# Optimization experiments

Measured on AMD Instinct MI355X. Metric: run time of the kernel, lower is better.

## Reference

```python
import jax, jax.numpy as jnp
import numpy as np

N_NODES = 100000
N_EDGES = 625000
HIDDEN = 128
N_LAYERS = 4
NUM_GRAPHS = 512
INPUT_DIM = 28
EDGE_DIM = 4
OUT_DIM = 1


def setup_inputs() -> dict:
    key = jax.random.key(0)
    ks = jax.random.split(key, 16)
    x = jax.random.randint(ks[0], (N_NODES, 1), 0, INPUT_DIM)
    edge_index = jax.random.randint(ks[1], (2, N_EDGES), 0, N_NODES)
    edge_attr = jax.random.randint(ks[2], (N_EDGES,), 0, EDGE_DIM)
    batch = jnp.sort(jax.random.randint(ks[3], (N_NODES,), 0, NUM_GRAPHS))
    s = 1.0 / np.sqrt(HIDDEN)
    node_emb = jax.random.normal(ks[4], (INPUT_DIM, HIDDEN), jnp.float32)
    edge_emb = jax.random.normal(ks[5], (EDGE_DIM, HIDDEN), jnp.float32)
    conv_W1 = jax.random.normal(ks[6], (N_LAYERS, HIDDEN, HIDDEN), jnp.float32) * s
    conv_b1 = jnp.zeros((N_LAYERS, HIDDEN), jnp.float32)
    conv_W2 = jax.random.normal(ks[7], (N_LAYERS, HIDDEN, HIDDEN), jnp.float32) * s
    conv_b2 = jnp.zeros((N_LAYERS, HIDDEN), jnp.float32)
    mlp_W1 = jax.random.normal(ks[8], (HIDDEN, HIDDEN // 2), jnp.float32) * s
    mlp_b1 = jnp.zeros((HIDDEN // 2,), jnp.float32)
    mlp_W2 = jax.random.normal(ks[9], (HIDDEN // 2, HIDDEN // 4), jnp.float32) * (1.0 / np.sqrt(HIDDEN // 2))
    mlp_b2 = jnp.zeros((HIDDEN // 4,), jnp.float32)
    mlp_W3 = jax.random.normal(ks[10], (HIDDEN // 4, OUT_DIM), jnp.float32) * (1.0 / np.sqrt(HIDDEN // 4))
    mlp_b3 = jnp.zeros((OUT_DIM,), jnp.float32)
    return dict(x=x, edge_index=edge_index, edge_attr=edge_attr, batch=batch,
                node_emb=node_emb, edge_emb=edge_emb,
                conv_W1=conv_W1, conv_b1=conv_b1, conv_W2=conv_W2, conv_b2=conv_b2,
                mlp_W1=mlp_W1, mlp_b1=mlp_b1, mlp_W2=mlp_W2, mlp_b2=mlp_b2,
                mlp_W3=mlp_W3, mlp_b3=mlp_b3)


def reference(x, edge_index, edge_attr, batch, node_emb, edge_emb,
              conv_W1, conv_b1, conv_W2, conv_b2,
              mlp_W1, mlp_b1, mlp_W2, mlp_b2, mlp_W3, mlp_b3):
    h = node_emb[x[:, 0]]                    # [N, H] embedding lookup (x.squeeze(-1))
    _attr = edge_emb[edge_attr]              # computed in original forward but unused by GINConv
    src, dst = edge_index[0], edge_index[1]
    for l in range(N_LAYERS):
        # GINConv (eps=0): mlp((1+eps)*x + sum_{j->i} x_j)
        agg = jax.ops.segment_sum(h[src], dst, num_segments=N_NODES)  # [N, H]
        z = agg + h
        z = jax.nn.relu(z @ conv_W1[l] + conv_b1[l])
        h = z @ conv_W2[l] + conv_b2[l]
    g = jax.ops.segment_sum(h, batch, num_segments=NUM_GRAPHS)        # global_add_pool [G, H]
    g = jax.nn.relu(g @ mlp_W1 + mlp_b1)
    g = jax.nn.relu(g @ mlp_W2 + mlp_b2)
    return g @ mlp_W3 + mlp_b3               # [G, 1]
```

## Files before the change

kernel.cpp:

```cpp
#include <hip/hip_runtime.h>

#define N_NODES 100000
#define N_EDGES 625000
#define HIDDEN 128
#define NUM_GRAPHS 512
#define CAP 40
#define PADN 100096

#define BUILD_BLKS 2443
#define EMBED_BLKS 6250
#define WT_BLKS 64

typedef unsigned int uint;
typedef unsigned short ushort;
typedef short v8s __attribute__((ext_vector_type(8)));
typedef float v16f __attribute__((ext_vector_type(16)));

__device__ __forceinline__ float b2f_lo(uint u) { return __uint_as_float(u << 16); }
__device__ __forceinline__ float b2f_hi(uint u) { return __uint_as_float(u & 0xffff0000u); }
__device__ __forceinline__ uint f2b(float f) {
  uint u = __float_as_uint(f);
  return (u + 0x7fffu + ((u >> 16) & 1u)) >> 16;
}

__global__ __launch_bounds__(256) void prep_k(const int* __restrict__ src,
                                              const int* __restrict__ dst,
                                              int* __restrict__ cursor,
                                              int* __restrict__ slots,
                                              const int* __restrict__ x,
                                              const float* __restrict__ emb,
                                              ushort* __restrict__ h,
                                              const float* __restrict__ W1,
                                              const float* __restrict__ W2,
                                              ushort* __restrict__ Wt) {
  int blk = blockIdx.x;
  int tid = threadIdx.x;
  if (blk < BUILD_BLKS) {
    int e = blk * 256 + tid;
    if (e < N_EDGES) {
      int d = dst[e];
      int p = atomicAdd(&cursor[d], 1);
      if (p < CAP) slots[(size_t)d * CAP + p] = src[e];
    }
  } else if (blk < BUILD_BLKS + EMBED_BLKS) {
    int t = (blk - BUILD_BLKS) * 256 + tid;
    int n = t >> 4;
    if (n < N_NODES) {
      int c = t & 15;
      const float4* e4 = (const float4*)(emb + (size_t)x[n] * HIDDEN + c * 8);
      float4 a = e4[0], b = e4[1];
      uint4 o;
      o.x = f2b(a.x) | (f2b(a.y) << 16);
      o.y = f2b(a.z) | (f2b(a.w) << 16);
      o.z = f2b(b.x) | (f2b(b.y) << 16);
      o.w = f2b(b.z) | (f2b(b.w) << 16);
      ((uint4*)h)[t] = o;
    }
  } else {
    int wb = blk - BUILD_BLKS - EMBED_BLKS;
    int mat = wb >> 3, chunk = wb & 7;
    const float* W = ((mat & 1) ? W2 : W1) + (size_t)(mat >> 1) * 16384;
    ushort* o = Wt + (size_t)mat * 16384;
#pragma unroll
    for (int jj = 0; jj < 8; jj++) {
      int idx = chunk * 2048 + tid + 256 * jj;
      int k = idx >> 7, n = idx & 127;
      int c = n >> 5, l31 = n & 31;
      int ks = k >> 4, khalf = (k >> 3) & 1, e = k & 7;
      o[(((c * 8 + ks) << 6) + (khalf << 5) + l31) * 8 + e] = (ushort)f2b(W[idx]);
    }
  }
}

__global__ __launch_bounds__(256) void hist_k(const int* __restrict__ cursor,
                                              int* __restrict__ bins) {
  __shared__ int lb[CAP + 1];
  int tid = threadIdx.x;
  if (tid <= CAP) lb[tid] = 0;
  __syncthreads();
  int n = blockIdx.x * 256 + tid;
  if (n < N_NODES) {
    int d = cursor[n]; if (d > CAP) d = CAP;
    atomicAdd(&lb[d], 1);
  }
  __syncthreads();
  if (tid <= CAP && lb[tid] > 0) atomicAdd(&bins[tid], lb[tid]);
}

__global__ __launch_bounds__(64) void scan_k(int* __restrict__ bins) {
  int i = threadIdx.x;
  int c = (i <= CAP) ? bins[i] : 0;
  int incl = c;
#pragma unroll
  for (int off = 1; off < 64; off <<= 1) {
    int t = __shfl_up(incl, off, 64);
    if (i >= off) incl += t;
  }
  if (i <= CAP) bins[i] = incl - c;
}

__global__ __launch_bounds__(256) void scatter_k(const int* __restrict__ cursor,
                                                 int* __restrict__ bins,
                                                 int* __restrict__ perm) {
  __shared__ int lb[CAP + 1];
  __shared__ int lbase[CAP + 1];
  int tid = threadIdx.x;
  if (tid <= CAP) lb[tid] = 0;
  __syncthreads();
  int n = blockIdx.x * 256 + tid;
  int d = 0, rank = 0;
  bool real = (n < N_NODES);
  if (real) {
    d = cursor[n]; if (d > CAP) d = CAP;
    rank = atomicAdd(&lb[d], 1);
  }
  __syncthreads();
  if (tid <= CAP) {
    int c = lb[tid];
    lbase[tid] = c > 0 ? atomicAdd(&bins[tid], c) : 0;
  }
  __syncthreads();
  if (real) perm[(N_NODES - 1) - (lbase[d] + rank)] = n;
  else if (n < PADN) perm[n] = 0;
}

union U { uint4 u; v8s s; };

__device__ __forceinline__ void loadrow(uint4 dst[8], const uint4* __restrict__ rowp,
                                        int khalf) {
#pragma unroll
  for (int ks = 0; ks < 8; ks++) dst[ks] = rowp[khalf + 2 * ks];
}

__device__ __forceinline__ void accum8(const uint4 u[8], float acc[8][8]) {
#pragma unroll
  for (int ks = 0; ks < 8; ks++) {
    acc[ks][0] += b2f_lo(u[ks].x); acc[ks][1] += b2f_hi(u[ks].x);
    acc[ks][2] += b2f_lo(u[ks].y); acc[ks][3] += b2f_hi(u[ks].y);
    acc[ks][4] += b2f_lo(u[ks].z); acc[ks][5] += b2f_hi(u[ks].z);
    acc[ks][6] += b2f_lo(u[ks].w); acc[ks][7] += b2f_hi(u[ks].w);
  }
}

__global__ __launch_bounds__(64, 3) void layer_k(const ushort* __restrict__ hin,
                                                 const int* __restrict__ cursor,
                                                 const int* __restrict__ slots,
                                                 const int* __restrict__ perm,
                                                 const ushort* __restrict__ W1f,
                                                 const ushort* __restrict__ W2f,
                                                 const float* __restrict__ b1,
                                                 const float* __restrict__ b2,
                                                 ushort* __restrict__ hout) {
  int lane = threadIdx.x;
  int l31 = lane & 31;
  int khalf = lane >> 5;
  int tb = blockIdx.x * 32;
  int prow = perm[tb + l31];
  bool valid = (tb + l31) < N_NODES;

  float acc[8][8];
#pragma unroll
  for (int ks = 0; ks < 8; ks++)
#pragma unroll
    for (int e = 0; e < 8; e++) acc[ks][e] = 0.f;

  const uint4* base = (const uint4*)hin;
  uint4 A[8], B[8];
  loadrow(A, base + (size_t)prow * 16, khalf);

  int deg = valid ? cursor[prow] : 0;
  if (deg > CAP) deg = CAP;
  const int* sl = slots + (size_t)prow * CAP;
  if (deg > 0) loadrow(B, base + (size_t)sl[0] * 16, khalf);
  __builtin_amdgcn_sched_barrier(0);
  accum8(A, acc);

  int j = 0;
  while (j + 2 <= deg) {
    loadrow(A, base + (size_t)sl[j + 1] * 16, khalf);
    __builtin_amdgcn_sched_barrier(0);
    accum8(B, acc);
    if (j + 2 < deg) loadrow(B, base + (size_t)sl[j + 2] * 16, khalf);
    __builtin_amdgcn_sched_barrier(0);
    accum8(A, acc);
    j += 2;
  }
  if (j < deg) accum8(B, acc);

  U afr[8];
#pragma unroll
  for (int ks = 0; ks < 8; ks++) {
    afr[ks].u.x = f2b(acc[ks][0]) | (f2b(acc[ks][1]) << 16);
    afr[ks].u.y = f2b(acc[ks][2]) | (f2b(acc[ks][3]) << 16);
    afr[ks].u.z = f2b(acc[ks][4]) | (f2b(acc[ks][5]) << 16);
    afr[ks].u.w = f2b(acc[ks][6]) | (f2b(acc[ks][7]) << 16);
  }

  const uint4* W1v = (const uint4*)W1f;
  v16f acc1[4] = {};
#pragma unroll
  for (int c = 0; c < 4; c++)
#pragma unroll
    for (int ks = 0; ks < 8; ks++) {
      U b; b.u = W1v[((c * 8 + ks) << 6) + lane];
      acc1[c] = __builtin_amdgcn_mfma_f32_32x32x16_bf16(b.s, afr[ks].s, acc1[c], 0, 0, 0);
    }

  uint u[4][4][2];
#pragma unroll
  for (int c = 0; c < 4; c++)
#pragma unroll
    for (int b = 0; b < 4; b++)
#pragma unroll
      for (int ap = 0; ap < 2; ap++) {
        int r0 = 2 * ap + 4 * b, r1 = r0 + 1;
        float v0 = fmaxf(acc1[c][r0] + b1[c * 32 + 2 * ap + 8 * b + 4 * khalf], 0.f);
        float v1 = fmaxf(acc1[c][r1] + b1[c * 32 + 2 * ap + 1 + 8 * b + 4 * khalf], 0.f);
        u[c][b][ap] = f2b(v0) | (f2b(v1) << 16);
      }

  uint got[4][2][2];
#pragma unroll
  for (int c = 0; c < 4; c++)
#pragma unroll
    for (int bh = 0; bh < 2; bh++)
#pragma unroll
      for (int ap = 0; ap < 2; ap++) {
        uint send = khalf ? u[c][2 * bh][ap] : u[c][2 * bh + 1][ap];
        got[c][bh][ap] = __shfl_xor(send, 32, 64);
      }

  U az[8];
#pragma unroll
  for (int ks = 0; ks < 8; ks++) {
    uint o0 = khalf ? u[ks >> 1][2 * (ks & 1) + 1][0] : u[ks >> 1][2 * (ks & 1)][0];
    uint o1 = khalf ? u[ks >> 1][2 * (ks & 1) + 1][1] : u[ks >> 1][2 * (ks & 1)][1];
    uint g0 = got[ks >> 1][ks & 1][0];
    uint g1 = got[ks >> 1][ks & 1][1];
    az[ks].u.x = khalf ? g0 : o0;
    az[ks].u.y = khalf ? g1 : o1;
    az[ks].u.z = khalf ? o0 : g0;
    az[ks].u.w = khalf ? o1 : g1;
  }

  const uint4* W2v = (const uint4*)W2f;
  v16f acc2[4] = {};
#pragma unroll
  for (int c = 0; c < 4; c++)
#pragma unroll
    for (int ks = 0; ks < 8; ks++) {
      U b; b.u = W2v[((c * 8 + ks) << 6) + lane];
      acc2[c] = __builtin_amdgcn_mfma_f32_32x32x16_bf16(az[ks].s, b.s, acc2[c], 0, 0, 0);
    }

  int trow[16];
#pragma unroll
  for (int r = 0; r < 16; r++) {
    int m = (r & 3) + 8 * (r >> 2) + 4 * khalf;
    trow[r] = __shfl(prow, m, 64);
  }
  float bv2[4];
#pragma unroll
  for (int c = 0; c < 4; c++) bv2[c] = b2[c * 32 + l31];
#pragma unroll
  for (int c = 0; c < 4; c++) {
    int col = c * 32 + l31;
#pragma unroll
    for (int r = 0; r < 16; r++) {
      int m = (r & 3) + 8 * (r >> 2) + 4 * khalf;
      if (tb + m < N_NODES)
        hout[(size_t)trow[r] * HIDDEN + col] = (ushort)f2b(acc2[c][r] + bv2[c]);
    }
  }
}

__global__ __launch_bounds__(256) void poolmlp_k(const ushort* __restrict__ h,
                                                 const int* __restrict__ batch,
                                                 const float* __restrict__ W1, const float* __restrict__ b1,
                                                 const float* __restrict__ W2, const float* __restrict__ b2,
                                                 const float* __restrict__ W3, const float* __restrict__ b3,
                                                 float* __restrict__ out) {
  __shared__ int se[2];
  __shared__ float red[16][16][8];
  __shared__ float gl[128];
  __shared__ float r2[64];
  __shared__ float r3[32];
  int gi = blockIdx.x, tid = threadIdx.x;
  if (tid < 2) {
    int target = gi + tid;
    int lo = 0, hi = N_NODES;
    while (lo < hi) {
      int mid = (lo + hi) >> 1;
      if (batch[mid] < target) lo = mid + 1; else hi = mid;
    }
    se[tid] = lo;
  }
  __syncthreads();
  int start = se[0], end = se[1];
  int cg = tid & 15, rg = tid >> 4;
  float acc[8] = {0.f, 0.f, 0.f, 0.f, 0.f, 0.f, 0.f, 0.f};
  for (int r = start + rg; r < end; r += 16) {
    uint4 v = ((const uint4*)h)[r * 16 + cg];
    acc[0] += b2f_lo(v.x); acc[1] += b2f_hi(v.x);
    acc[2] += b2f_lo(v.y); acc[3] += b2f_hi(v.y);
    acc[4] += b2f_lo(v.z); acc[5] += b2f_hi(v.z);
    acc[6] += b2f_lo(v.w); acc[7] += b2f_hi(v.w);
  }
#pragma unroll
  for (int j = 0; j < 8; j++) red[rg][cg][j] = acc[j];
  __syncthreads();
  if (rg == 0) {
    float s[8];
#pragma unroll
    for (int j = 0; j < 8; j++) s[j] = red[0][cg][j];
#pragma unroll
    for (int i = 1; i < 16; i++)
#pragma unroll
      for (int j = 0; j < 8; j++) s[j] += red[i][cg][j];
#pragma unroll
    for (int j = 0; j < 8; j++) gl[cg * 8 + j] = s[j];
  }
  __syncthreads();
  if (tid < 64) {
    float s = b1[tid];
    for (int k = 0; k < 128; k++) s = fmaf(gl[k], W1[k * 64 + tid], s);
    r2[tid] = fmaxf(s, 0.f);
  }
  __syncthreads();
  if (tid < 32) {
    float s2 = b2[tid];
    for (int k = 0; k < 64; k++) s2 = fmaf(r2[k], W2[k * 32 + tid], s2);
    r3[tid] = fmaxf(s2, 0.f);
  }
  __syncthreads();
  if (tid < 64) {
    float pv = (tid < 32) ? r3[tid] * W3[tid] : 0.f;
#pragma unroll
    for (int off = 32; off > 0; off >>= 1) pv += __shfl_down(pv, off);
    if (tid == 0) out[gi] = pv + b3[0];
  }
}

extern "C" void kernel_launch(void* const* d_in, const int* in_sizes, int n_in,
                              void* d_out, int out_size, void* d_ws, size_t ws_size,
                              hipStream_t stream) {
  const int* x = (const int*)d_in[0];
  const int* src = (const int*)d_in[1];
  const int* dst = src + N_EDGES;
  const int* batch = (const int*)d_in[3];
  const float* node_emb = (const float*)d_in[4];
  const float* cW1 = (const float*)d_in[6];
  const float* cb1 = (const float*)d_in[7];
  const float* cW2 = (const float*)d_in[8];
  const float* cb2 = (const float*)d_in[9];
  const float* mW1 = (const float*)d_in[10];
  const float* mb1 = (const float*)d_in[11];
  const float* mW2 = (const float*)d_in[12];
  const float* mb2 = (const float*)d_in[13];
  const float* mW3 = (const float*)d_in[14];
  const float* mb3 = (const float*)d_in[15];
  float* out = (float*)d_out;

  char* p = (char*)d_ws;
  const size_t HB = (size_t)N_NODES * HIDDEN * sizeof(ushort);
  ushort* h = (ushort*)p;      p += HB;
  ushort* t0 = (ushort*)p;     p += HB;
  ushort* Wtb = (ushort*)p;    p += (size_t)8 * 16384 * sizeof(ushort);
  int* cursor = (int*)p;       p += (size_t)N_NODES * sizeof(int);
  int* bins = (int*)p;         p += 64 * sizeof(int);
  int* slots = (int*)p;        p += (size_t)N_NODES * CAP * sizeof(int);
  int* perm = (int*)p;         p += (size_t)PADN * sizeof(int);

  (void)hipMemsetAsync(cursor, 0, ((size_t)N_NODES + 64) * sizeof(int), stream);
  prep_k<<<BUILD_BLKS + EMBED_BLKS + WT_BLKS, 256, 0, stream>>>(
      src, dst, cursor, slots, x, node_emb, h, cW1, cW2, Wtb);
  hist_k<<<PADN / 256, 256, 0, stream>>>(cursor, bins);
  scan_k<<<1, 64, 0, stream>>>(bins);
  scatter_k<<<PADN / 256, 256, 0, stream>>>(cursor, bins, perm);

  const int grid = PADN / 32;
  ushort* bufs[2] = {h, t0};
  for (int l = 0; l < 4; l++) {
    layer_k<<<grid, 64, 0, stream>>>(bufs[l & 1], cursor, slots, perm,
                                     Wtb + (size_t)(2 * l) * 16384,
                                     Wtb + (size_t)(2 * l + 1) * 16384,
                                     cb1 + (size_t)l * HIDDEN,
                                     cb2 + (size_t)l * HIDDEN,
                                     bufs[(l & 1) ^ 1]);
  }
  poolmlp_k<<<NUM_GRAPHS, 256, 0, stream>>>(h, batch, mW1, mb1, mW2, mb2, mW3, mb3, out);
}
```

Baseline: 341.1 us.

## Split neighbor aggregation across two wavefronts with LDS reduction

The layer kernel now launches 128 threads per block: two wavefronts each gather alternate neighbors of the same 32 nodes, and the second wave's partial sums are reduced through shared memory before only the first wave runs the MFMA MLP. Neighbor slot indices are prefetched as int4 vectors instead of scalar loads. This is meant to halve the serial gather latency chain per node and raise memory-level parallelism. The costs are a 16KB LDS buffer, a block barrier, an idle second wave during the GEMM phase, and lower occupancy pressure trade-offs.

Result: slower. 563.7 us (+65.3%).

```diff
diff --git a/kernel.cpp b/kernel.cpp
--- a/kernel.cpp
+++ b/kernel.cpp
@@ -142,16 +142,19 @@
   }
 }
 
-__global__ __launch_bounds__(64, 3) void layer_k(const ushort* __restrict__ hin,
-                                                 const int* __restrict__ cursor,
-                                                 const int* __restrict__ slots,
-                                                 const int* __restrict__ perm,
-                                                 const ushort* __restrict__ W1f,
-                                                 const ushort* __restrict__ W2f,
-                                                 const float* __restrict__ b1,
-                                                 const float* __restrict__ b2,
-                                                 ushort* __restrict__ hout) {
-  int lane = threadIdx.x;
+__global__ __launch_bounds__(128, 4) void layer_k(const ushort* __restrict__ hin,
+                                                  const int* __restrict__ cursor,
+                                                  const int* __restrict__ slots,
+                                                  const int* __restrict__ perm,
+                                                  const ushort* __restrict__ W1f,
+                                                  const ushort* __restrict__ W2f,
+                                                  const float* __restrict__ b1,
+                                                  const float* __restrict__ b2,
+                                                  ushort* __restrict__ hout) {
+  __shared__ float red[64 * 64];
+  int tid = threadIdx.x;
+  int wid = tid >> 6;
+  int lane = tid & 63;
   int l31 = lane & 31;
   int khalf = lane >> 5;
   int tb = blockIdx.x * 32;
@@ -166,26 +169,64 @@
 
   const uint4* base = (const uint4*)hin;
   uint4 A[8], B[8];
-  loadrow(A, base + (size_t)prow * 16, khalf);
 
   int deg = valid ? cursor[prow] : 0;
   if (deg > CAP) deg = CAP;
-  const int* sl = slots + (size_t)prow * CAP;
-  if (deg > 0) loadrow(B, base + (size_t)sl[0] * 16, khalf);
-  __builtin_amdgcn_sched_barrier(0);
-  accum8(A, acc);
-
-  int j = 0;
-  while (j + 2 <= deg) {
-    loadrow(A, base + (size_t)sl[j + 1] * 16, khalf);
+  bool need2 = __ballot(deg > 1) != 0ull;
+
+  const int4* slv = (const int4*)(slots + (size_t)prow * CAP);
+  int mg = (deg - wid + 1) >> 1;
+  int4 ck = slv[0];
+  int4 cn = slv[1];
+
+  if (wid == 0) {
+    loadrow(A, base + (size_t)prow * 16, khalf);
+    if (mg > 0) loadrow(B, base + (size_t)ck.x * 16, khalf);
+    __builtin_amdgcn_sched_barrier(0);
+    accum8(A, acc);
+  } else {
+    if (mg > 0) loadrow(B, base + (size_t)ck.y * 16, khalf);
+    __builtin_amdgcn_sched_barrier(0);
+  }
+
+  int i = 0;
+  while (i + 2 <= mg) {
+    int sA = wid ? ck.w : ck.z;
+    loadrow(A, base + (size_t)sA * 16, khalf);
     __builtin_amdgcn_sched_barrier(0);
     accum8(B, acc);
-    if (j + 2 < deg) loadrow(B, base + (size_t)sl[j + 2] * 16, khalf);
+    int cidx = (i >> 1) + 2;
+    if (cidx > 9) cidx = 9;
+    int4 nx = slv[cidx];
+    if (i + 2 < mg) {
+      int sB = wid ? cn.y : cn.x;
+      loadrow(B, base + (size_t)sB * 16, khalf);
+    }
     __builtin_amdgcn_sched_barrier(0);
     accum8(A, acc);
-    j += 2;
-  }
-  if (j < deg) accum8(B, acc);
+    ck = cn; cn = nx;
+    i += 2;
+  }
+  if (i < mg) accum8(B, acc);
+
+  if (need2) {
+    if (wid == 1) {
+#pragma unroll
+      for (int ks = 0; ks < 8; ks++)
+#pragma unroll
+        for (int e = 0; e < 8; e++)
+          red[(ks * 8 + e) * 64 + lane] = acc[ks][e];
+    }
+    __syncthreads();
+    if (wid == 0) {
+#pragma unroll
+      for (int ks = 0; ks < 8; ks++)
+#pragma unroll
+        for (int e = 0; e < 8; e++)
+          acc[ks][e] += red[(ks * 8 + e) * 64 + lane];
+    }
+  }
+  if (wid == 1) return;
 
   U afr[8];
 #pragma unroll
@@ -381,12 +422,12 @@
   const int grid = PADN / 32;
   ushort* bufs[2] = {h, t0};
   for (int l = 0; l < 4; l++) {
-    layer_k<<<grid, 64, 0, stream>>>(bufs[l & 1], cursor, slots, perm,
-                                     Wtb + (size_t)(2 * l) * 16384,
-                                     Wtb + (size_t)(2 * l + 1) * 16384,
-                                     cb1 + (size_t)l * HIDDEN,
-                                     cb2 + (size_t)l * HIDDEN,
-                                     bufs[(l & 1) ^ 1]);
+    layer_k<<<grid, 128, 0, stream>>>(bufs[l & 1], cursor, slots, perm,
+                                      Wtb + (size_t)(2 * l) * 16384,
+                                      Wtb + (size_t)(2 * l + 1) * 16384,
+                                      cb1 + (size_t)l * HIDDEN,
+                                      cb2 + (size_t)l * HIDDEN,
+                                      bufs[(l & 1) ^ 1]);
   }
   poolmlp_k<<<NUM_GRAPHS, 256, 0, stream>>>(h, batch, mW1, mb1, mW2, mb2, mW3, mb3, out);
 }
```

## Split fused GIN layer into gather-aggregate kernel and in-place MLP GEMM kernel

Applied to the files above, without the earlier changes.

Each layer's fused gather+MLP kernel is split into two kernels. The new aggregation kernel puts 8 lanes on each node, each loading two 16-byte chunks, and prefetches neighbor indices as int4 with a four-deep pipeline of row loads. A separate GEMM kernel then reads the aggregated rows in natural order and writes the MLP output in place. This aims to improve memory-level parallelism and occupancy in the gather phase, at the cost of an extra write and read of the full node feature array and an extra launch per layer.

New measurement: 358.9 us. 5.2% more time.

```diff
diff --git a/kernel.cpp b/kernel.cpp
--- a/kernel.cpp
+++ b/kernel.cpp
@@ -126,15 +126,15 @@
 
 union U { uint4 u; v8s s; };
 
-__device__ __forceinline__ void loadrow(uint4 dst[8], const uint4* __restrict__ rowp,
-                                        int khalf) {
-#pragma unroll
-  for (int ks = 0; ks < 8; ks++) dst[ks] = rowp[khalf + 2 * ks];
-}
-
-__device__ __forceinline__ void accum8(const uint4 u[8], float acc[8][8]) {
-#pragma unroll
-  for (int ks = 0; ks < 8; ks++) {
+__device__ __forceinline__ void loadrow2(uint4 dst[2], const uint4* __restrict__ rowp,
+                                         int q) {
+  dst[0] = rowp[q];
+  dst[1] = rowp[q + 8];
+}
+
+__device__ __forceinline__ void accum2(const uint4 u[2], float acc[2][8]) {
+#pragma unroll
+  for (int ks = 0; ks < 2; ks++) {
     acc[ks][0] += b2f_lo(u[ks].x); acc[ks][1] += b2f_hi(u[ks].x);
     acc[ks][2] += b2f_lo(u[ks].y); acc[ks][3] += b2f_hi(u[ks].y);
     acc[ks][4] += b2f_lo(u[ks].z); acc[ks][5] += b2f_hi(u[ks].z);
@@ -142,59 +142,94 @@
   }
 }
 
-__global__ __launch_bounds__(64, 3) void layer_k(const ushort* __restrict__ hin,
-                                                 const int* __restrict__ cursor,
-                                                 const int* __restrict__ slots,
-                                                 const int* __restrict__ perm,
-                                                 const ushort* __restrict__ W1f,
-                                                 const ushort* __restrict__ W2f,
-                                                 const float* __restrict__ b1,
-                                                 const float* __restrict__ b2,
-                                                 ushort* __restrict__ hout) {
+__global__ __launch_bounds__(256, 5) void agg_k(const ushort* __restrict__ hin,
+                                                const int* __restrict__ cursor,
+                                                const int* __restrict__ slots,
+                                                const int* __restrict__ perm,
+                                                ushort* __restrict__ t1) {
+  int tid = threadIdx.x;
+  int lane = tid & 63;
+  int w = blockIdx.x * 4 + (tid >> 6);
+  int r8 = lane & 7;
+  int q = lane >> 3;
+  int pidx = w * 8 + r8;
+  bool valid = pidx < N_NODES;
+  int prow = valid ? perm[pidx] : 0;
+  int deg = valid ? cursor[prow] : 0;
+  if (deg > CAP) deg = CAP;
+  const int4* slv = (const int4*)(slots + (size_t)prow * CAP);
+  const uint4* base = (const uint4*)hin;
+
+  float acc[2][8];
+#pragma unroll
+  for (int ks = 0; ks < 2; ks++)
+#pragma unroll
+    for (int e = 0; e < 8; e++) acc[ks][e] = 0.f;
+
+  uint4 P0[2], P1[2], P2[2], P3[2];
+  int4 ck = slv[0];
+  int4 cn = slv[1];
+
+  loadrow2(P3, base + (size_t)prow * 16, q);
+  if (deg > 0) loadrow2(P0, base + (size_t)ck.x * 16, q);
+  if (deg > 1) loadrow2(P1, base + (size_t)ck.y * 16, q);
+  if (deg > 2) loadrow2(P2, base + (size_t)ck.z * 16, q);
+  __builtin_amdgcn_sched_barrier(0);
+  accum2(P3, acc);
+
+  int j = 0;
+  while (j + 4 <= deg) {
+    loadrow2(P3, base + (size_t)ck.w * 16, q);
+    __builtin_amdgcn_sched_barrier(0);
+    accum2(P0, acc);
+    int ni = (j >> 2) + 2; if (ni > 9) ni = 9;
+    int4 nx = slv[ni];
+    if (j + 4 < deg) loadrow2(P0, base + (size_t)cn.x * 16, q);
+    __builtin_amdgcn_sched_barrier(0);
+    accum2(P1, acc);
+    if (j + 5 < deg) loadrow2(P1, base + (size_t)cn.y * 16, q);
+    __builtin_amdgcn_sched_barrier(0);
+    accum2(P2, acc);
+    if (j + 6 < deg) loadrow2(P2, base + (size_t)cn.z * 16, q);
+    __builtin_amdgcn_sched_barrier(0);
+    accum2(P3, acc);
+    ck = cn; cn = nx;
+    j += 4;
+  }
+  if (j < deg)     accum2(P0, acc);
+  if (j + 1 < deg) accum2(P1, acc);
+  if (j + 2 < deg) accum2(P2, acc);
+
+  if (valid) {
+    uint4 o0, o1;
+    o0.x = f2b(acc[0][0]) | (f2b(acc[0][1]) << 16);
+    o0.y = f2b(acc[0][2]) | (f2b(acc[0][3]) << 16);
+    o0.z = f2b(acc[0][4]) | (f2b(acc[0][5]) << 16);
+    o0.w = f2b(acc[0][6]) | (f2b(acc[0][7]) << 16);
+    o1.x = f2b(acc[1][0]) | (f2b(acc[1][1]) << 16);
+    o1.y = f2b(acc[1][2]) | (f2b(acc[1][3]) << 16);
+    o1.z = f2b(acc[1][4]) | (f2b(acc[1][5]) << 16);
+    o1.w = f2b(acc[1][6]) | (f2b(acc[1][7]) << 16);
+    uint4* orow = (uint4*)(t1 + (size_t)prow * HIDDEN);
+    orow[q] = o0;
+    orow[q + 8] = o1;
+  }
+}
+
+__global__ __launch_bounds__(64, 3) void gemm_k(ushort* __restrict__ t,
+                                                const ushort* __restrict__ W1f,
+                                                const ushort* __restrict__ W2f,
+                                                const float* __restrict__ b1,
+                                                const float* __restrict__ b2) {
   int lane = threadIdx.x;
   int l31 = lane & 31;
   int khalf = lane >> 5;
-  int tb = blockIdx.x * 32;
-  int prow = perm[tb + l31];
-  bool valid = (tb + l31) < N_NODES;
-
-  float acc[8][8];
-#pragma unroll
-  for (int ks = 0; ks < 8; ks++)
-#pragma unroll
-    for (int e = 0; e < 8; e++) acc[ks][e] = 0.f;
-
-  const uint4* base = (const uint4*)hin;
-  uint4 A[8], B[8];
-  loadrow(A, base + (size_t)prow * 16, khalf);
-
-  int deg = valid ? cursor[prow] : 0;
-  if (deg > CAP) deg = CAP;
-  const int* sl = slots + (size_t)prow * CAP;
-  if (deg > 0) loadrow(B, base + (size_t)sl[0] * 16, khalf);
-  __builtin_amdgcn_sched_barrier(0);
-  accum8(A, acc);
-
-  int j = 0;
-  while (j + 2 <= deg) {
-    loadrow(A, base + (size_t)sl[j + 1] * 16, khalf);
-    __builtin_amdgcn_sched_barrier(0);
-    accum8(B, acc);
-    if (j + 2 < deg) loadrow(B, base + (size_t)sl[j + 2] * 16, khalf);
-    __builtin_amdgcn_sched_barrier(0);
-    accum8(A, acc);
-    j += 2;
-  }
-  if (j < deg) accum8(B, acc);
-
+  int rb = blockIdx.x * 32;
+
+  const uint4* rowp = (const uint4*)t + (size_t)(rb + l31) * 16;
   U afr[8];
 #pragma unroll
-  for (int ks = 0; ks < 8; ks++) {
-    afr[ks].u.x = f2b(acc[ks][0]) | (f2b(acc[ks][1]) << 16);
-    afr[ks].u.y = f2b(acc[ks][2]) | (f2b(acc[ks][3]) << 16);
-    afr[ks].u.z = f2b(acc[ks][4]) | (f2b(acc[ks][5]) << 16);
-    afr[ks].u.w = f2b(acc[ks][6]) | (f2b(acc[ks][7]) << 16);
-  }
+  for (int ks = 0; ks < 8; ks++) afr[ks].u = rowp[khalf + 2 * ks];
 
   const uint4* W1v = (const uint4*)W1f;
   v16f acc1[4] = {};
@@ -253,12 +288,6 @@
       acc2[c] = __builtin_amdgcn_mfma_f32_32x32x16_bf16(az[ks].s, b.s, acc2[c], 0, 0, 0);
     }
 
-  int trow[16];
-#pragma unroll
-  for (int r = 0; r < 16; r++) {
-    int m = (r & 3) + 8 * (r >> 2) + 4 * khalf;
-    trow[r] = __shfl(prow, m, 64);
-  }
   float bv2[4];
 #pragma unroll
   for (int c = 0; c < 4; c++) bv2[c] = b2[c * 32 + l31];
@@ -268,8 +297,7 @@
 #pragma unroll
     for (int r = 0; r < 16; r++) {
       int m = (r & 3) + 8 * (r >> 2) + 4 * khalf;
-      if (tb + m < N_NODES)
-        hout[(size_t)trow[r] * HIDDEN + col] = (ushort)f2b(acc2[c][r] + bv2[c]);
+      t[(size_t)(rb + m) * HIDDEN + col] = (ushort)f2b(acc2[c][r] + bv2[c]);
     }
   }
 }
@@ -378,15 +406,16 @@
   scan_k<<<1, 64, 0, stream>>>(bins);
   scatter_k<<<PADN / 256, 256, 0, stream>>>(cursor, bins, perm);
 
-  const int grid = PADN / 32;
   ushort* bufs[2] = {h, t0};
   for (int l = 0; l < 4; l++) {
-    layer_k<<<grid, 64, 0, stream>>>(bufs[l & 1], cursor, slots, perm,
-                                     Wtb + (size_t)(2 * l) * 16384,
-                                     Wtb + (size_t)(2 * l + 1) * 16384,
-                                     cb1 + (size_t)l * HIDDEN,
-                                     cb2 + (size_t)l * HIDDEN,
-                                     bufs[(l & 1) ^ 1]);
+    ushort* in = bufs[l & 1];
+    ushort* tmp = bufs[(l & 1) ^ 1];
+    agg_k<<<PADN / 32, 256, 0, stream>>>(in, cursor, slots, perm, tmp);
+    gemm_k<<<N_NODES / 32, 64, 0, stream>>>(tmp,
+                                            Wtb + (size_t)(2 * l) * 16384,
+                                            Wtb + (size_t)(2 * l + 1) * 16384,
+                                            cb1 + (size_t)l * HIDDEN,
+                                            cb2 + (size_t)l * HIDDEN);
   }
   poolmlp_k<<<NUM_GRAPHS, 256, 0, stream>>>(h, batch, mW1, mb1, mW2, mb2, mW3, mb3, out);
 }
```

## Remap gather so 8 lanes share each row, exchange via LDS

Applied to the files above, without the earlier changes.

The neighbor-gather phase now has 8 lanes cooperate on each node row, each loading 32 contiguous bytes, and every lane handles 4 nodes instead of one half-row of one node. This is meant to improve memory coalescing of the scattered row loads and add memory-level parallelism. The accumulated sums are converted to bf16 and written to a padded shared-memory buffer, then read back in the MFMA fragment layout. The cost is extra LDS traffic, more divergence from differing per-node degrees (the loop runs to the max degree of 4 nodes), and higher register pressure. There is no barrier between the LDS writes and reads, but the block is a single 64-lane wavefront, so this is likely fine.

New measurement: 374.6 us. 1.1x slower.

```diff
diff --git a/kernel.cpp b/kernel.cpp
--- a/kernel.cpp
+++ b/kernel.cpp
@@ -126,19 +126,23 @@
 
 union U { uint4 u; v8s s; };
 
-__device__ __forceinline__ void loadrow(uint4 dst[8], const uint4* __restrict__ rowp,
-                                        int khalf) {
-#pragma unroll
-  for (int ks = 0; ks < 8; ks++) dst[ks] = rowp[khalf + 2 * ks];
-}
-
-__device__ __forceinline__ void accum8(const uint4 u[8], float acc[8][8]) {
-#pragma unroll
-  for (int ks = 0; ks < 8; ks++) {
-    acc[ks][0] += b2f_lo(u[ks].x); acc[ks][1] += b2f_hi(u[ks].x);
-    acc[ks][2] += b2f_lo(u[ks].y); acc[ks][3] += b2f_hi(u[ks].y);
-    acc[ks][4] += b2f_lo(u[ks].z); acc[ks][5] += b2f_hi(u[ks].z);
-    acc[ks][6] += b2f_lo(u[ks].w); acc[ks][7] += b2f_hi(u[ks].w);
+__device__ __forceinline__ void acc_set(const uint4 u[2], float a[16]) {
+#pragma unroll
+  for (int k = 0; k < 2; k++) {
+    a[k * 8 + 0] = b2f_lo(u[k].x); a[k * 8 + 1] = b2f_hi(u[k].x);
+    a[k * 8 + 2] = b2f_lo(u[k].y); a[k * 8 + 3] = b2f_hi(u[k].y);
+    a[k * 8 + 4] = b2f_lo(u[k].z); a[k * 8 + 5] = b2f_hi(u[k].z);
+    a[k * 8 + 6] = b2f_lo(u[k].w); a[k * 8 + 7] = b2f_hi(u[k].w);
+  }
+}
+
+__device__ __forceinline__ void acc_add(const uint4 u[2], float a[16]) {
+#pragma unroll
+  for (int k = 0; k < 2; k++) {
+    a[k * 8 + 0] += b2f_lo(u[k].x); a[k * 8 + 1] += b2f_hi(u[k].x);
+    a[k * 8 + 2] += b2f_lo(u[k].y); a[k * 8 + 3] += b2f_hi(u[k].y);
+    a[k * 8 + 4] += b2f_lo(u[k].z); a[k * 8 + 5] += b2f_hi(u[k].z);
+    a[k * 8 + 6] += b2f_lo(u[k].w); a[k * 8 + 7] += b2f_hi(u[k].w);
   }
 }
 
@@ -151,50 +155,103 @@
                                                  const float* __restrict__ b1,
                                                  const float* __restrict__ b2,
                                                  ushort* __restrict__ hout) {
+  __shared__ uint4 xchv[32 * 17];
   int lane = threadIdx.x;
+  int q = lane & 7;
+  int r8 = lane >> 3;
+  int tb = blockIdx.x * 32;
+
+  int prow[4], deg[4];
+#pragma unroll
+  for (int g = 0; g < 4; g++) {
+    int idx = tb + g * 8 + r8;
+    bool v = idx < N_NODES;
+    prow[g] = v ? perm[idx] : 0;
+    int d = v ? cursor[prow[g]] : 0;
+    if (d > CAP) d = CAP;
+    deg[g] = d;
+  }
+  const uint4* base = (const uint4*)hin;
+
+  float acc[4][16];
+  uint4 A[4][2], B[4][2];
+  int sj1[4];
+
+#pragma unroll
+  for (int g = 0; g < 4; g++) {
+    const uint4* rp = base + (size_t)prow[g] * 16 + q * 2;
+    A[g][0] = rp[0]; A[g][1] = rp[1];
+  }
+#pragma unroll
+  for (int g = 0; g < 4; g++) {
+    if (deg[g] > 0) {
+      int s0 = slots[(size_t)prow[g] * CAP];
+      const uint4* rp = base + (size_t)s0 * 16 + q * 2;
+      B[g][0] = rp[0]; B[g][1] = rp[1];
+    }
+    sj1[g] = (deg[g] > 1) ? slots[(size_t)prow[g] * CAP + 1] : 0;
+  }
+  __builtin_amdgcn_sched_barrier(0);
+#pragma unroll
+  for (int g = 0; g < 4; g++) acc_set(A[g], acc[g]);
+
+  int md = max(max(deg[0], deg[1]), max(deg[2], deg[3]));
+  int j = 0;
+  while (j + 2 <= md) {
+#pragma unroll
+    for (int g = 0; g < 4; g++)
+      if (j + 1 < deg[g]) {
+        const uint4* rp = base + (size_t)sj1[g] * 16 + q * 2;
+        A[g][0] = rp[0]; A[g][1] = rp[1];
+      }
+    int sj2[4];
+#pragma unroll
+    for (int g = 0; g < 4; g++)
+      sj2[g] = (j + 2 < deg[g]) ? slots[(size_t)prow[g] * CAP + j + 2] : 0;
+    __builtin_amdgcn_sched_barrier(0);
+#pragma unroll
+    for (int g = 0; g < 4; g++) if (j < deg[g]) acc_add(B[g], acc[g]);
+#pragma unroll
+    for (int g = 0; g < 4; g++)
+      if (j + 2 < deg[g]) {
+        const uint4* rp = base + (size_t)sj2[g] * 16 + q * 2;
+        B[g][0] = rp[0]; B[g][1] = rp[1];
+      }
+#pragma unroll
+    for (int g = 0; g < 4; g++)
+      sj1[g] = (j + 3 < deg[g]) ? slots[(size_t)prow[g] * CAP + j + 3] : 0;
+    __builtin_amdgcn_sched_barrier(0);
+#pragma unroll
+    for (int g = 0; g < 4; g++) if (j + 1 < deg[g]) acc_add(A[g], acc[g]);
+    j += 2;
+  }
+  if (j < md) {
+#pragma unroll
+    for (int g = 0; g < 4; g++) if (j < deg[g]) acc_add(B[g], acc[g]);
+  }
+
+#pragma unroll
+  for (int g = 0; g < 4; g++) {
+    int row = g * 8 + r8;
+    uint4 o0, o1;
+    o0.x = f2b(acc[g][0])  | (f2b(acc[g][1])  << 16);
+    o0.y = f2b(acc[g][2])  | (f2b(acc[g][3])  << 16);
+    o0.z = f2b(acc[g][4])  | (f2b(acc[g][5])  << 16);
+    o0.w = f2b(acc[g][6])  | (f2b(acc[g][7])  << 16);
+    o1.x = f2b(acc[g][8])  | (f2b(acc[g][9])  << 16);
+    o1.y = f2b(acc[g][10]) | (f2b(acc[g][11]) << 16);
+    o1.z = f2b(acc[g][12]) | (f2b(acc[g][13]) << 16);
+    o1.w = f2b(acc[g][14]) | (f2b(acc[g][15]) << 16);
+    xchv[row * 17 + 2 * q] = o0;
+    xchv[row * 17 + 2 * q + 1] = o1;
+  }
+
   int l31 = lane & 31;
   int khalf = lane >> 5;
-  int tb = blockIdx.x * 32;
-  int prow = perm[tb + l31];
-  bool valid = (tb + l31) < N_NODES;
-
-  float acc[8][8];
+  U afr[8];
 #pragma unroll
   for (int ks = 0; ks < 8; ks++)
-#pragma unroll
-    for (int e = 0; e < 8; e++) acc[ks][e] = 0.f;
-
-  const uint4* base = (const uint4*)hin;
-  uint4 A[8], B[8];
-  loadrow(A, base + (size_t)prow * 16, khalf);
-
-  int deg = valid ? cursor[prow] : 0;
-  if (deg > CAP) deg = CAP;
-  const int* sl = slots + (size_t)prow * CAP;
-  if (deg > 0) loadrow(B, base + (size_t)sl[0] * 16, khalf);
-  __builtin_amdgcn_sched_barrier(0);
-  accum8(A, acc);
-
-  int j = 0;
-  while (j + 2 <= deg) {
-    loadrow(A, base + (size_t)sl[j + 1] * 16, khalf);
-    __builtin_amdgcn_sched_barrier(0);
-    accum8(B, acc);
-    if (j + 2 < deg) loadrow(B, base + (size_t)sl[j + 2] * 16, khalf);
-    __builtin_amdgcn_sched_barrier(0);
-    accum8(A, acc);
-    j += 2;
-  }
-  if (j < deg) accum8(B, acc);
-
-  U afr[8];
-#pragma unroll
-  for (int ks = 0; ks < 8; ks++) {
-    afr[ks].u.x = f2b(acc[ks][0]) | (f2b(acc[ks][1]) << 16);
-    afr[ks].u.y = f2b(acc[ks][2]) | (f2b(acc[ks][3]) << 16);
-    afr[ks].u.z = f2b(acc[ks][4]) | (f2b(acc[ks][5]) << 16);
-    afr[ks].u.w = f2b(acc[ks][6]) | (f2b(acc[ks][7]) << 16);
-  }
+    afr[ks].u = xchv[l31 * 17 + 2 * ks + khalf];
 
   const uint4* W1v = (const uint4*)W1f;
   v16f acc1[4] = {};
@@ -253,11 +310,12 @@
       acc2[c] = __builtin_amdgcn_mfma_f32_32x32x16_bf16(az[ks].s, b.s, acc2[c], 0, 0, 0);
     }
 
+  int prowst = perm[tb + l31];
   int trow[16];
 #pragma unroll
   for (int r = 0; r < 16; r++) {
     int m = (r & 3) + 8 * (r >> 2) + 4 * khalf;
-    trow[r] = __shfl(prow, m, 64);
+    trow[r] = __shfl(prowst, m, 64);
   }
   float bv2[4];
 #pragma unroll
```
